# Kernel tuning notes

Hardware: AMD Instinct MI355X
Metric: run time of the kernel (lower is better)

## Reference

```python
import jax, jax.numpy as jnp
import numpy as np

N, E, DIN, GB, GD, LB, LD, G = 50000, 640000, 64, 128, 4, 256, 2, 1024


def setup_inputs() -> dict:
    key = jax.random.key(0)
    ks = jax.random.split(key, 20)
    p = lambda k, shape: (jax.random.normal(k, shape, dtype=jnp.float32) * 0.05)
    return {
        "x": jax.random.normal(ks[0], (N, DIN), dtype=jnp.float32),
        "edge_index": jax.random.randint(ks[1], (2, E), 0, N, dtype=jnp.int64),
        "batch": jnp.sort(jax.random.randint(ks[2], (N,), 0, G, dtype=jnp.int64)),
        "num_graphs": G,
        "W0": p(ks[3], (DIN, GB)), "b0": p(ks[4], (GB,)),
        "Wg": p(ks[5], (GD, GB, GB)), "bg": p(ks[6], (GD, GB)),
        "gamma_g": jnp.ones((GD, GB), jnp.float32), "beta_g": jnp.zeros((GD, GB), jnp.float32),
        "Wl0": p(ks[7], (GB, LB)), "bl0": p(ks[8], (LB,)),
        "Wl": p(ks[9], (LD, LB, LB)), "bl": p(ks[10], (LD, LB)),
        "gamma_l": jnp.ones((LD, LB), jnp.float32), "beta_l": jnp.zeros((LD, LB), jnp.float32),
        "Wout": p(ks[11], (LB, 2)), "bout": p(ks[12], (2,)),
    }


def reference(x, edge_index, batch, num_graphs, W0, b0, Wg, bg, gamma_g, beta_g,
              Wl0, bl0, Wl, bl, gamma_l, beta_l, Wout, bout):
    n = x.shape[0]
    src, dst = edge_index[0], edge_index[1]
    # GCN degree normalization with self loops: deg = 1 + in-degree
    deg = jax.ops.segment_sum(jnp.ones(src.shape[0], x.dtype), dst, num_segments=n) + 1.0
    dinv = jax.lax.rsqrt(deg)                 # deg^{-1/2}
    enorm = dinv[src] * dinv[dst]             # [E] edge norm
    snorm = dinv * dinv                       # [N] self-loop norm (deg^{-1})

    def gcn(h, W, b):
        hw = h @ W                                            # [N, GB]
        agg = jax.ops.segment_sum(hw[src] * enorm[:, None], dst, num_segments=n)
        return agg + hw * snorm[:, None] + b

    def bn(h, g, bt):  # training-mode batchnorm (biased var), eps=1e-5
        m = h.mean(0)
        v = h.var(0)
        return (h - m) * jax.lax.rsqrt(v + 1e-5) * g + bt

    h = jax.nn.relu(gcn(x, W0, b0))
    for i in range(Wg.shape[0]):
        h = jax.nn.relu(bn(gcn(h, Wg[i], bg[i]), gamma_g[i], beta_g[i]))
    # global_add_pool
    hp = jax.ops.segment_sum(h, batch, num_segments=num_graphs)  # [G, GB]
    h = jax.nn.relu(hp @ Wl0 + bl0)
    for i in range(Wl.shape[0]):
        h = jax.nn.relu(bn(h @ Wl[i] + bl[i], gamma_l[i], beta_l[i]))
    return h @ Wout + bout
```

## Files before the change

### kernel.cpp

```cpp
#include <hip/hip_runtime.h>

#define NN 50000
#define EE 640000
#define DINv 64
#define GBv 128
#define GDv 4
#define LBv 256
#define LDv 2
#define GGv 1024

#define NB 196
#define BCAP 4096
#define BTILE 4096
#define NBT ((EE + BTILE - 1) / BTILE)

#define NTILES ((NN + 63) / 64)
#define UPN (NN * 16)
#define CONVN (DINv * GBv + GDv * GBv * GBv)

typedef _Float16 f16x8 __attribute__((ext_vector_type(8)));
typedef float f32x4 __attribute__((ext_vector_type(4)));

__device__ __forceinline__ float h2f(ushort u) {
  union { ushort u; _Float16 h; } x;
  x.u = u;
  return (float)x.h;
}
__device__ __forceinline__ ushort f2h(float f) {
  union { ushort u; _Float16 h; } x;
  x.h = (_Float16)f;
  return x.u;
}


__global__ __launch_bounds__(256) void k_bucket(const int* __restrict__ ei,
                                                int* __restrict__ bcnt,
                                                uint* __restrict__ bkt) {
  __shared__ int lcnt[NB];
  __shared__ int lbase[NB];
  __shared__ int gbase[NB];
  __shared__ int ls[256];
  __shared__ uint stage[BTILE];
  __shared__ ushort sb[BTILE];
  int tid = threadIdx.x;
  int t0 = blockIdx.x * BTILE;
  int cnt = min(BTILE, EE - t0);
  for (int i = tid; i < NB; i += 256) lcnt[i] = 0;
  __syncthreads();

  uint en[16];
  int bb[16], rk[16];
  int nper = (cnt + 255) >> 8;
  for (int k = 0; k < nper; k++) {
    int e = k * 256 + tid;
    if (e < cnt) {
      int src = ei[t0 + e];
      int dst = ei[EE + t0 + e];
      int b = dst >> 8;
      en[k] = ((uint)src << 8) | (uint)(dst & 255);
      bb[k] = b;
      rk[k] = atomicAdd(&lcnt[b], 1);
    } else {
      bb[k] = -1;
    }
  }
  __syncthreads();

  int v = (tid < NB) ? lcnt[tid] : 0;
  ls[tid] = v;
  __syncthreads();
  for (int off = 1; off < 256; off <<= 1) {
    int t = (tid >= off) ? ls[tid - off] : 0;
    __syncthreads();
    ls[tid] += t;
    __syncthreads();
  }
  if (tid < NB) {
    lbase[tid] = ls[tid] - v;
    gbase[tid] = atomicAdd(&bcnt[tid], v);
  }
  __syncthreads();

  for (int k = 0; k < nper; k++) {
    if (bb[k] >= 0) {
      int slot = lbase[bb[k]] + rk[k];
      stage[slot] = en[k];
      sb[slot] = (ushort)bb[k];
    }
  }
  __syncthreads();

  for (int i = tid; i < cnt; i += 256) {
    int b = sb[i];
    bkt[(size_t)b * BCAP + gbase[b] + (i - lbase[b])] = stage[i];
  }
}

__global__ __launch_bounds__(256) void k_bscan(const int* __restrict__ bcnt,
                                               int* __restrict__ bbase,
                                               int* __restrict__ offs) {
  __shared__ int ls[256];
  int tid = threadIdx.x;
  int v = (tid < NB) ? bcnt[tid] : 0;
  ls[tid] = v;
  __syncthreads();
  for (int off = 1; off < 256; off <<= 1) {
    int t = (tid >= off) ? ls[tid - off] : 0;
    __syncthreads();
    ls[tid] += t;
    __syncthreads();
  }
  if (tid < NB) bbase[tid] = ls[tid] - v;
  if (tid == 0) offs[NN] = EE;
}


__global__ __launch_bounds__(256) void k_csr(const uint* __restrict__ bkt,
                                             const int* __restrict__ bcnt,
                                             const int* __restrict__ bbase,
                                             int* __restrict__ offs,
                                             float* __restrict__ dinv,
                                             int* __restrict__ col,
                                             int* __restrict__ deg,
                                             int* __restrict__ ghist) {
  __shared__ int lhist[256];
  __shared__ int lofs[256];
  __shared__ int lcur[256];
  __shared__ int lh2[64];
  int b = blockIdx.x;
  int cnt = bcnt[b], base = bbase[b];
  const uint* B = bkt + (size_t)b * BCAP;
  int tid = threadIdx.x;
  lhist[tid] = 0;
  if (tid < 64) lh2[tid] = 0;
  __syncthreads();
  for (int i = tid; i < cnt; i += 256) atomicAdd(&lhist[B[i] & 255], 1);
  __syncthreads();
  int v = lhist[tid];
  lofs[tid] = v;
  __syncthreads();
  for (int off = 1; off < 256; off <<= 1) {
    int t = (tid >= off) ? lofs[tid - off] : 0;
    __syncthreads();
    lofs[tid] += t;
    __syncthreads();
  }
  int excl = lofs[tid] - v;
  int n = b * 256 + tid;
  if (n < NN) {
    offs[n] = base + excl;
    dinv[n] = rsqrtf((float)(v + 1));
    int d = min(v, 63);
    deg[n] = d;
    atomicAdd(&lh2[d], 1);
  }
  lcur[tid] = excl;
  __syncthreads();
  if (tid < 64 && lh2[tid]) atomicAdd(&ghist[tid], lh2[tid]);
  for (int i = tid; i < cnt; i += 256) {
    uint e = B[i];
    int p = atomicAdd(&lcur[e & 255], 1);
    col[base + p] = (int)(e >> 8);
  }
}

__global__ void k_dscan(const int* __restrict__ ghist, int* __restrict__ dcur) {
  if (threadIdx.x == 0 && blockIdx.x == 0) {
    int run = 0;
    for (int i = 0; i < 64; i++) {
      dcur[i] = run;
      run += ghist[i];
    }
  }
}

__global__ __launch_bounds__(256) void k_dperm(const int* __restrict__ deg,
                                               int* __restrict__ dcur,
                                               int* __restrict__ perm) {
  __shared__ int lhist[64];
  __shared__ int lbase[64];
  int tid = threadIdx.x;
  if (tid < 64) lhist[tid] = 0;
  __syncthreads();
  int n = blockIdx.x * 256 + tid;
  int d = 0, rk = 0;
  if (n < NN) {
    d = deg[n];
    rk = atomicAdd(&lhist[d], 1);
  }
  __syncthreads();
  if (tid < 64 && lhist[tid]) lbase[tid] = atomicAdd(&dcur[tid], lhist[tid]);
  __syncthreads();
  if (n < NN) perm[lbase[d] + rk] = n;
}


__global__ __launch_bounds__(256) void k_prep(const float* __restrict__ x,
                                              const float* __restrict__ dinv,
                                              const float* __restrict__ W0,
                                              const float* __restrict__ Wg,
                                              ushort* __restrict__ u,
                                              ushort* __restrict__ Wt0,
                                              ushort* __restrict__ Wtg) {
  int idx = blockIdx.x * 256 + threadIdx.x;
  if (idx < UPN) {
    int n = idx >> 4;
    float4 v = ((const float4*)x)[idx];
    float d = dinv[n];
    union { ushort us[4]; uint2 q; } o;
    o.us[0] = f2h(v.x * d);
    o.us[1] = f2h(v.y * d);
    o.us[2] = f2h(v.z * d);
    o.us[3] = f2h(v.w * d);
    ((uint2*)u)[idx] = o.q;
  } else {
    int j = idx - UPN;
    if (j < DINv * GBv) {
      int c = j >> 6, k = j & 63;
      Wt0[j] = f2h(W0[k * GBv + c]);
    } else if (j < CONVN) {
      int e = j - DINv * GBv;
      int i = e >> 14, rem = e & 16383;
      int c = rem >> 7, k = rem & 127;
      Wtg[e] = f2h(Wg[i * GBv * GBv + k * GBv + c]);
    }
  }
}


template <int K, int MODE>
__global__ __launch_bounds__(256) void k_agg(const ushort* __restrict__ Gin,
                                             const int* __restrict__ col,
                                             const int* __restrict__ offs,
                                             const float* __restrict__ dinv,
                                             const int* __restrict__ perm,
                                             const float* __restrict__ st,
                                             const float* __restrict__ gamma,
                                             const float* __restrict__ beta,
                                             ushort* __restrict__ V) {
  constexpr int VEC = K / 16;
  __shared__ float sS[128], sT[128];
  int tid = threadIdx.x;
  if constexpr (MODE == 2) {
    if (tid < 128) {
      float mu = st[tid] * (1.f / NN);
      float var = st[128 + tid] * (1.f / NN) - mu * mu;
      float s = rsqrtf(var + 1e-5f) * gamma[tid];
      sS[tid] = s;
      sT[tid] = beta[tid] - mu * s;
    }
    __syncthreads();
  }
  int lane = tid & 63;
  int q = lane >> 4, m = lane & 15;
  int idx = blockIdx.x * 16 + (tid >> 6) * 4 + q;
  int n = perm[idx];

  float sc[VEC], tc[VEC];
  if constexpr (MODE == 2) {
#pragma unroll
    for (int v = 0; v < VEC; v++) {
      sc[v] = sS[m * VEC + v];
      tc[v] = sT[m * VEC + v];
    }
  }

  union U { uint4 v4; uint2 v2; ushort us[8]; };
  auto loadrow = [&](int s) {
    U u;
    const ushort* p = Gin + (long)s * K + m * VEC;
    if constexpr (VEC == 8) u.v4 = *(const uint4*)p;
    else u.v2 = *(const uint2*)p;
    return u;
  };
  float acc[VEC];
#pragma unroll
  for (int v = 0; v < VEC; v++) acc[v] = 0.f;
  auto addrow = [&](U u, float dv) {
#pragma unroll
    for (int v = 0; v < VEC; v++) {
      float g = h2f(u.us[v]);
      if constexpr (MODE == 0) acc[v] += g;
      else if constexpr (MODE == 1) acc[v] += fmaxf(g, 0.f) * dv;
      else acc[v] += fmaxf(g * sc[v] + tc[v], 0.f) * dv;
    }
  };

  float dn = dinv[n];
  addrow(loadrow(n), dn);

  int s0 = offs[n], s1 = offs[n + 1];
  int j = s0;
  for (; j + 7 < s1; j += 8) {
    int si[8];
#pragma unroll
    for (int t = 0; t < 8; t++) si[t] = col[j + t];
    U uu[8];
#pragma unroll
    for (int t = 0; t < 8; t++) uu[t] = loadrow(si[t]);
    float dd[8];
#pragma unroll
    for (int t = 0; t < 8; t++) dd[t] = (MODE != 0) ? dinv[si[t]] : 0.f;
#pragma unroll
    for (int t = 0; t < 8; t++) addrow(uu[t], dd[t]);
  }
  for (; j + 3 < s1; j += 4) {
    int si[4];
#pragma unroll
    for (int t = 0; t < 4; t++) si[t] = col[j + t];
    U uu[4];
#pragma unroll
    for (int t = 0; t < 4; t++) uu[t] = loadrow(si[t]);
    float dd[4];
#pragma unroll
    for (int t = 0; t < 4; t++) dd[t] = (MODE != 0) ? dinv[si[t]] : 0.f;
#pragma unroll
    for (int t = 0; t < 4; t++) addrow(uu[t], dd[t]);
  }
  for (; j < s1; j++) {
    int s = col[j];
    U u = loadrow(s);
    float dv = (MODE != 0) ? dinv[s] : 0.f;
    addrow(u, dv);
  }

  U o;
#pragma unroll
  for (int v = 0; v < VEC; v++) o.us[v] = f2h(acc[v] * dn);
  ushort* op = V + (long)n * K + m * VEC;
  if constexpr (VEC == 8) *(uint4*)op = o.v4;
  else *(uint2*)op = o.v2;
}


template <int K, bool STATS>
__global__ __launch_bounds__(256) void k_mm(const ushort* __restrict__ X,
                                            const ushort* __restrict__ Wt,
                                            const float* __restrict__ bias,
                                            float* __restrict__ stG,
                                            ushort* __restrict__ Gout) {
  constexpr int KP = K + 8;
  constexpr int CP = 136;
  constexpr bool REUSE = (K == 128);
  __shared__ __attribute__((aligned(16))) _Float16 sW[128 * KP];
  __shared__ __attribute__((aligned(16))) _Float16 sA[64 * KP];
  __shared__ __attribute__((aligned(16))) _Float16 sCbuf[REUSE ? 8 : 64 * CP];
  __shared__ float sB[128];
  __shared__ float ssum[128], ssq[128];
  _Float16* sC = REUSE ? sA : sCbuf;
  int tid = threadIdx.x;

  {
    constexpr int CH = K / 8;
    for (int i = tid; i < 128 * CH; i += 256) {
      int c = i / CH, ch = i - c * CH;
      *(uint4*)&sW[c * KP + ch * 8] = ((const uint4*)Wt)[i];
    }
  }
  if (tid < 128) {
    sB[tid] = bias[tid];
    if constexpr (STATS) {
      ssum[tid] = 0.f;
      ssq[tid] = 0.f;
    }
  }

  int w = tid >> 6, lane = tid & 63;
  int m = lane & 15, quad = lane >> 4;
  int crow = 16 * w + quad * 4;

  float ps[8], pq[8];
  if constexpr (STATS) {
#pragma unroll
    for (int ct = 0; ct < 8; ct++) { ps[ct] = 0.f; pq[ct] = 0.f; }
  }

  for (int tile = blockIdx.x; tile < NTILES; tile += gridDim.x) {
    int row0 = tile * 64;
    __syncthreads();

    {
      int r = tid >> 2, col0 = (tid & 3) * (K / 4);
      int gr = row0 + r;
      const uint4* p = (const uint4*)(X + (long)gr * K + col0);
#pragma unroll
      for (int ch = 0; ch < K / 32; ch++) {
        uint4 v = (gr < NN) ? p[ch] : make_uint4(0, 0, 0, 0);
        *(uint4*)&sA[r * KP + col0 + ch * 8] = v;
      }
    }
    __syncthreads();

    f32x4 acc[8];
#pragma unroll
    for (int ct = 0; ct < 8; ct++) acc[ct] = (f32x4){0.f, 0.f, 0.f, 0.f};
    const _Float16* pa = &sA[(16 * w + m) * KP + quad * 8];
#pragma unroll
    for (int ks = 0; ks < K; ks += 32) {
      f16x8 a = *(const f16x8*)(pa + ks);
#pragma unroll
      for (int ct = 0; ct < 8; ct++) {
        f16x8 b = *(const f16x8*)&sW[(ct * 16 + m) * KP + ks + quad * 8];
        acc[ct] = __builtin_amdgcn_mfma_f32_16x16x32_f16(a, b, acc[ct], 0, 0, 0);
      }
    }

    if constexpr (STATS) {
#pragma unroll
      for (int ct = 0; ct < 8; ct++) {
        int c = ct * 16 + m;
        float b = sB[c];
#pragma unroll
        for (int r = 0; r < 4; r++) {
          if (row0 + crow + r < NN) {
            float g = acc[ct][r] + b;
            ps[ct] += g;
            pq[ct] += g * g;
          }
        }
      }
    }
    if constexpr (REUSE) __syncthreads();

#pragma unroll
    for (int ct = 0; ct < 8; ct++) {
      int c = ct * 16 + m;
      float b = sB[c];
#pragma unroll
      for (int r = 0; r < 4; r++) sC[(crow + r) * CP + c] = (_Float16)(acc[ct][r] + b);
    }
    __syncthreads();

    {
      int r = tid >> 2, col0 = (tid & 3) * 32;
      int gr = row0 + r;
      if (gr < NN) {
        const uint4* src = (const uint4*)&sC[r * CP + col0];
        uint4* dst = (uint4*)(Gout + (long)gr * 128 + col0);
#pragma unroll
        for (int ch = 0; ch < 4; ch++) dst[ch] = src[ch];
      }
    }
  }

  if constexpr (STATS) {
#pragma unroll
    for (int ct = 0; ct < 8; ct++) {
      float s = ps[ct], q = pq[ct];
      s += __shfl_xor(s, 16);
      q += __shfl_xor(q, 16);
      s += __shfl_xor(s, 32);
      q += __shfl_xor(q, 32);
      if (quad == 0) {
        atomicAdd(&ssum[ct * 16 + m], s);
        atomicAdd(&ssq[ct * 16 + m], q);
      }
    }
    __syncthreads();
    if (tid < 128) {
      int c = (tid + blockIdx.x * 8) & 127;
      atomicAdd(&stG[c], ssum[c]);
      atomicAdd(&stG[128 + c], ssq[c]);
    }
  }
}


__global__ __launch_bounds__(128) void k_pool2(const ushort* __restrict__ G,
                                               const float* __restrict__ st,
                                               const float* __restrict__ gamma,
                                               const float* __restrict__ beta,
                                               const int* __restrict__ batch,
                                               float* __restrict__ hp) {
  __shared__ int sse[2];
  int g = blockIdx.x;
  int c = threadIdx.x;
  if (c < 2) {
    int key = g + c;
    int lo = 0, hi = NN;
    while (lo < hi) {
      int mid = (lo + hi) >> 1;
      if (batch[mid] < key) lo = mid + 1;
      else hi = mid;
    }
    sse[c] = lo;
  }
  __syncthreads();
  int s = sse[0], e = sse[1];
  float m = st[c] * (1.f / NN);
  float v = st[128 + c] * (1.f / NN) - m * m;
  float sc = rsqrtf(v + 1e-5f) * gamma[c];
  float tc = beta[c] - m * sc;
  float acc = 0.f;
  for (int n = s; n < e; n++) acc += fmaxf(h2f(G[(long)n * 128 + c]) * sc + tc, 0.f);
  hp[(long)g * 128 + c] = acc;
}


__global__ void k_colstats(const float* __restrict__ X, int rows, float* __restrict__ st) {
  int c = threadIdx.x;
  int C = blockDim.x;
  float s = 0.f, q = 0.f;
  for (int r = blockIdx.x; r < rows; r += gridDim.x) {
    float v = X[(long)r * C + c];
    s += v;
    q += v * v;
  }
  atomicAdd(&st[c], s);
  atomicAdd(&st[C + c], q);
}


template <int KIN, int MODE>
__global__ __launch_bounds__(256) void k_fc(const float* __restrict__ X,
                                            const float* __restrict__ W,
                                            const float* __restrict__ b,
                                            const float* __restrict__ st,
                                            const float* __restrict__ gamma,
                                            const float* __restrict__ beta,
                                            float* __restrict__ Y) {
  __shared__ float sx[KIN];
  int g = blockIdx.x;
  int c = threadIdx.x;
  for (int k = c; k < KIN; k += 256) {
    float v = X[(long)g * KIN + k];
    if constexpr (MODE == 2) {
      float m = st[k] * (1.f / GGv);
      float var = st[KIN + k] * (1.f / GGv) - m * m;
      v = fmaxf((v - m) * rsqrtf(var + 1e-5f) * gamma[k] + beta[k], 0.f);
    }
    sx[k] = v;
  }
  __syncthreads();
  float acc = b[c];
#pragma unroll 8
  for (int k = 0; k < KIN; k++) acc += sx[k] * W[(long)k * 256 + c];
  Y[(long)g * 256 + c] = (MODE == 0) ? fmaxf(acc, 0.f) : acc;
}

__global__ __launch_bounds__(256) void k_out(const float* __restrict__ X,
                                             const float* __restrict__ st,
                                             const float* __restrict__ gamma,
                                             const float* __restrict__ beta,
                                             const float* __restrict__ Wout,
                                             const float* __restrict__ bout,
                                             float* __restrict__ out) {
  int g = blockIdx.x * 4 + (threadIdx.x >> 6);
  int l = threadIdx.x & 63;
  float a0 = 0.f, a1 = 0.f;
  for (int k = l; k < LBv; k += 64) {
    float z = X[(long)g * LBv + k];
    float m = st[k] * (1.f / GGv);
    float var = st[LBv + k] * (1.f / GGv) - m * m;
    float x = fmaxf((z - m) * rsqrtf(var + 1e-5f) * gamma[k] + beta[k], 0.f);
    a0 += x * Wout[2 * k];
    a1 += x * Wout[2 * k + 1];
  }
  for (int off = 32; off > 0; off >>= 1) {
    a0 += __shfl_down(a0, off);
    a1 += __shfl_down(a1, off);
  }
  if (l == 0) {
    out[2 * g] = a0 + bout[0];
    out[2 * g + 1] = a1 + bout[1];
  }
}


extern "C" void kernel_launch(void* const* d_in, const int* in_sizes, int n_in,
                              void* d_out, int out_size, void* d_ws, size_t ws_size,
                              hipStream_t stream) {
  const float* x = (const float*)d_in[0];
  const int* ei = (const int*)d_in[1];
  const int* batch = (const int*)d_in[2];
  const float* W0 = (const float*)d_in[4];
  const float* b0 = (const float*)d_in[5];
  const float* Wg = (const float*)d_in[6];
  const float* bg = (const float*)d_in[7];
  const float* gamma_g = (const float*)d_in[8];
  const float* beta_g = (const float*)d_in[9];
  const float* Wl0 = (const float*)d_in[10];
  const float* bl0 = (const float*)d_in[11];
  const float* Wl = (const float*)d_in[12];
  const float* bl = (const float*)d_in[13];
  const float* gamma_l = (const float*)d_in[14];
  const float* beta_l = (const float*)d_in[15];
  const float* Wout = (const float*)d_in[16];
  const float* bout = (const float*)d_in[17];
  float* out = (float*)d_out;

  char* w = (char*)d_ws;
  auto alloc = [&](size_t bytes) {
    void* p = (void*)w;
    w += (bytes + 255) & ~(size_t)255;
    return p;
  };
  int* bcnt = (int*)alloc((size_t)NB * 4);
  float* stAll = (float*)alloc((size_t)(4 * 256 + 2 * 512) * 4);
  int* ghist = (int*)alloc((size_t)64 * 4);
  size_t zspan = (char*)w - (char*)bcnt;
  uint* bkt = (uint*)alloc((size_t)NB * BCAP * 4);
  int* bbase = (int*)alloc((size_t)NB * 4);
  int* offs = (int*)alloc((size_t)(NN + 1) * 4);
  int* col = (int*)alloc((size_t)EE * 4);
  float* dinv = (float*)alloc((size_t)NN * 4);
  int* deg = (int*)alloc((size_t)NN * 4);
  int* perm = (int*)alloc((size_t)NN * 4);
  int* dcur = (int*)alloc((size_t)64 * 4);
  ushort* u = (ushort*)alloc((size_t)NN * DINv * 2);
  ushort* V = (ushort*)alloc((size_t)NN * GBv * 2);
  ushort* g = (ushort*)alloc((size_t)NN * GBv * 2);
  ushort* Wt0 = (ushort*)alloc((size_t)DINv * GBv * 2);
  ushort* Wtg = (ushort*)alloc((size_t)GDv * GBv * GBv * 2);
  float* hp = (float*)alloc((size_t)GGv * GBv * 4);
  float* m1 = (float*)alloc((size_t)GGv * LBv * 4);
  float* m2 = (float*)alloc((size_t)GGv * LBv * 4);

  float* stg = stAll;
  float* sth0 = stAll + 4 * 256;
  float* sth1 = sth0 + 512;

  hipMemsetAsync(bcnt, 0, zspan, stream);

  k_bucket<<<NBT, 256, 0, stream>>>(ei, bcnt, bkt);
  k_bscan<<<1, 256, 0, stream>>>(bcnt, bbase, offs);
  k_csr<<<NB, 256, 0, stream>>>(bkt, bcnt, bbase, offs, dinv, col, deg, ghist);
  k_dscan<<<1, 64, 0, stream>>>(ghist, dcur);
  k_dperm<<<NB, 256, 0, stream>>>(deg, dcur, perm);
  k_prep<<<(UPN + CONVN + 255) / 256, 256, 0, stream>>>(x, dinv, W0, Wg, u, Wt0, Wtg);

  const int AGG = NN / 16;
  const int MMG = 512;

  k_agg<64, 0><<<AGG, 256, 0, stream>>>(u, col, offs, dinv, perm, nullptr, nullptr,
                                        nullptr, V);
  k_mm<64, false><<<MMG, 256, 0, stream>>>(V, Wt0, b0, nullptr, g);

  k_agg<128, 1><<<AGG, 256, 0, stream>>>(g, col, offs, dinv, perm, nullptr, nullptr,
                                         nullptr, V);
  k_mm<128, true><<<MMG, 256, 0, stream>>>(V, Wtg, bg, stg, g);

  for (int i = 1; i < GDv; i++) {
    k_agg<128, 2><<<AGG, 256, 0, stream>>>(g, col, offs, dinv, perm,
                                           stg + (size_t)(i - 1) * 256,
                                           gamma_g + (size_t)(i - 1) * GBv,
                                           beta_g + (size_t)(i - 1) * GBv, V);
    k_mm<128, true><<<MMG, 256, 0, stream>>>(V, Wtg + (size_t)i * GBv * GBv,
                                             bg + (size_t)i * GBv, stg + (size_t)i * 256, g);
  }

  k_pool2<<<GGv, 128, 0, stream>>>(g, stg + 3 * 256, gamma_g + 3 * GBv, beta_g + 3 * GBv,
                                   batch, hp);

  k_fc<GBv, 0><<<GGv, 256, 0, stream>>>(hp, Wl0, bl0, nullptr, nullptr, nullptr, m1);
  k_fc<LBv, 1><<<GGv, 256, 0, stream>>>(m1, Wl, bl, nullptr, nullptr, nullptr, m2);
  k_colstats<<<256, LBv, 0, stream>>>(m2, GGv, sth0);
  k_fc<LBv, 2><<<GGv, 256, 0, stream>>>(m2, Wl + (size_t)LBv * LBv, bl + LBv, sth0,
                                        gamma_l, beta_l, m1);
  k_colstats<<<256, LBv, 0, stream>>>(m1, GGv, sth1);
  k_out<<<GGv / 4, 256, 0, stream>>>(m1, sth1, gamma_l + LBv, beta_l + LBv, Wout, bout, out);
}
```

Before: 446.8 us.

## Fold tiny scan and column-stat kernels into neighbouring kernels to cut launches

The bucket-count scan is moved into every k_csr block, which now redundantly computes the prefix over all 196 bucket counts. The degree-histogram scan is moved into k_dperm, with the global offset added at write time. The two column-statistics kernels are replaced by atomic accumulation of sum and sum-of-squares inside the FC kernels. This removes four small serial launches at the cost of redundant per-block scans and 2x256 atomics per FC block, which contend on the same addresses.

Measured after the change: 473.8 us. 1.06x slower.

```diff
diff --git a/kernel.cpp b/kernel.cpp
--- a/kernel.cpp
+++ b/kernel.cpp
@@ -96,28 +96,9 @@
   }
 }
 
-__global__ __launch_bounds__(256) void k_bscan(const int* __restrict__ bcnt,
-                                               int* __restrict__ bbase,
-                                               int* __restrict__ offs) {
-  __shared__ int ls[256];
-  int tid = threadIdx.x;
-  int v = (tid < NB) ? bcnt[tid] : 0;
-  ls[tid] = v;
-  __syncthreads();
-  for (int off = 1; off < 256; off <<= 1) {
-    int t = (tid >= off) ? ls[tid - off] : 0;
-    __syncthreads();
-    ls[tid] += t;
-    __syncthreads();
-  }
-  if (tid < NB) bbase[tid] = ls[tid] - v;
-  if (tid == 0) offs[NN] = EE;
-}
-
 
 __global__ __launch_bounds__(256) void k_csr(const uint* __restrict__ bkt,
                                              const int* __restrict__ bcnt,
-                                             const int* __restrict__ bbase,
                                              int* __restrict__ offs,
                                              float* __restrict__ dinv,
                                              int* __restrict__ col,
@@ -127,13 +108,25 @@
   __shared__ int lofs[256];
   __shared__ int lcur[256];
   __shared__ int lh2[64];
+  __shared__ int sbase[256];
   int b = blockIdx.x;
-  int cnt = bcnt[b], base = bbase[b];
-  const uint* B = bkt + (size_t)b * BCAP;
   int tid = threadIdx.x;
+
+  int bv = (tid < NB) ? bcnt[tid] : 0;
+  sbase[tid] = bv;
   lhist[tid] = 0;
   if (tid < 64) lh2[tid] = 0;
   __syncthreads();
+  for (int off = 1; off < 256; off <<= 1) {
+    int t = (tid >= off) ? sbase[tid - off] : 0;
+    __syncthreads();
+    sbase[tid] += t;
+    __syncthreads();
+  }
+  int base = sbase[b] - bcnt[b];
+  int cnt = bcnt[b];
+  const uint* B = bkt + (size_t)b * BCAP;
+
   for (int i = tid; i < cnt; i += 256) atomicAdd(&lhist[B[i] & 255], 1);
   __syncthreads();
   int v = lhist[tid];
@@ -157,6 +150,7 @@
   lcur[tid] = excl;
   __syncthreads();
   if (tid < 64 && lh2[tid]) atomicAdd(&ghist[tid], lh2[tid]);
+  if (b == 0 && tid == 0) offs[NN] = EE;
   for (int i = tid; i < cnt; i += 256) {
     uint e = B[i];
     int p = atomicAdd(&lcur[e & 255], 1);
@@ -164,23 +158,22 @@
   }
 }
 
-__global__ void k_dscan(const int* __restrict__ ghist, int* __restrict__ dcur) {
-  if (threadIdx.x == 0 && blockIdx.x == 0) {
-    int run = 0;
-    for (int i = 0; i < 64; i++) {
-      dcur[i] = run;
-      run += ghist[i];
-    }
-  }
-}
-
 __global__ __launch_bounds__(256) void k_dperm(const int* __restrict__ deg,
-                                               int* __restrict__ dcur,
+                                               const int* __restrict__ ghist,
+                                               int* __restrict__ gcur,
                                                int* __restrict__ perm) {
   __shared__ int lhist[64];
   __shared__ int lbase[64];
+  __shared__ int gbase[64];
   int tid = threadIdx.x;
   if (tid < 64) lhist[tid] = 0;
+  if (tid == 0) {
+    int run = 0;
+    for (int i = 0; i < 64; i++) {
+      gbase[i] = run;
+      run += ghist[i];
+    }
+  }
   __syncthreads();
   int n = blockIdx.x * 256 + tid;
   int d = 0, rk = 0;
@@ -189,9 +182,9 @@
     rk = atomicAdd(&lhist[d], 1);
   }
   __syncthreads();
-  if (tid < 64 && lhist[tid]) lbase[tid] = atomicAdd(&dcur[tid], lhist[tid]);
-  __syncthreads();
-  if (n < NN) perm[lbase[d] + rk] = n;
+  if (tid < 64 && lhist[tid]) lbase[tid] = atomicAdd(&gcur[tid], lhist[tid]);
+  __syncthreads();
+  if (n < NN) perm[gbase[d] + lbase[d] + rk] = n;
 }
 
 
@@ -497,27 +490,14 @@
 }
 
 
-__global__ void k_colstats(const float* __restrict__ X, int rows, float* __restrict__ st) {
-  int c = threadIdx.x;
-  int C = blockDim.x;
-  float s = 0.f, q = 0.f;
-  for (int r = blockIdx.x; r < rows; r += gridDim.x) {
-    float v = X[(long)r * C + c];
-    s += v;
-    q += v * v;
-  }
-  atomicAdd(&st[c], s);
-  atomicAdd(&st[C + c], q);
-}
-
-
-template <int KIN, int MODE>
+template <int KIN, int MODE, bool STATS>
 __global__ __launch_bounds__(256) void k_fc(const float* __restrict__ X,
                                             const float* __restrict__ W,
                                             const float* __restrict__ b,
                                             const float* __restrict__ st,
                                             const float* __restrict__ gamma,
                                             const float* __restrict__ beta,
+                                            float* __restrict__ stOut,
                                             float* __restrict__ Y) {
   __shared__ float sx[KIN];
   int g = blockIdx.x;
@@ -535,7 +515,12 @@
   float acc = b[c];
 #pragma unroll 8
   for (int k = 0; k < KIN; k++) acc += sx[k] * W[(long)k * 256 + c];
-  Y[(long)g * 256 + c] = (MODE == 0) ? fmaxf(acc, 0.f) : acc;
+  float yv = (MODE == 0) ? fmaxf(acc, 0.f) : acc;
+  Y[(long)g * 256 + c] = yv;
+  if constexpr (STATS) {
+    atomicAdd(&stOut[c], yv);
+    atomicAdd(&stOut[256 + c], yv * yv);
+  }
 }
 
 __global__ __launch_bounds__(256) void k_out(const float* __restrict__ X,
@@ -598,15 +583,14 @@
   int* bcnt = (int*)alloc((size_t)NB * 4);
   float* stAll = (float*)alloc((size_t)(4 * 256 + 2 * 512) * 4);
   int* ghist = (int*)alloc((size_t)64 * 4);
+  int* gcur = (int*)alloc((size_t)64 * 4);
   size_t zspan = (char*)w - (char*)bcnt;
   uint* bkt = (uint*)alloc((size_t)NB * BCAP * 4);
-  int* bbase = (int*)alloc((size_t)NB * 4);
   int* offs = (int*)alloc((size_t)(NN + 1) * 4);
   int* col = (int*)alloc((size_t)EE * 4);
   float* dinv = (float*)alloc((size_t)NN * 4);
   int* deg = (int*)alloc((size_t)NN * 4);
   int* perm = (int*)alloc((size_t)NN * 4);
-  int* dcur = (int*)alloc((size_t)64 * 4);
   ushort* u = (ushort*)alloc((size_t)NN * DINv * 2);
   ushort* V = (ushort*)alloc((size_t)NN * GBv * 2);
   ushort* g = (ushort*)alloc((size_t)NN * GBv * 2);
@@ -623,10 +607,8 @@
   hipMemsetAsync(bcnt, 0, zspan, stream);
 
   k_bucket<<<NBT, 256, 0, stream>>>(ei, bcnt, bkt);
-  k_bscan<<<1, 256, 0, stream>>>(bcnt, bbase, offs);
-  k_csr<<<NB, 256, 0, stream>>>(bkt, bcnt, bbase, offs, dinv, col, deg, ghist);
-  k_dscan<<<1, 64, 0, stream>>>(ghist, dcur);
-  k_dperm<<<NB, 256, 0, stream>>>(deg, dcur, perm);
+  k_csr<<<NB, 256, 0, stream>>>(bkt, bcnt, offs, dinv, col, deg, ghist);
+  k_dperm<<<NB, 256, 0, stream>>>(deg, ghist, gcur, perm);
   k_prep<<<(UPN + CONVN + 255) / 256, 256, 0, stream>>>(x, dinv, W0, Wg, u, Wt0, Wtg);
 
   const int AGG = NN / 16;
@@ -652,11 +634,11 @@
   k_pool2<<<GGv, 128, 0, stream>>>(g, stg + 3 * 256, gamma_g + 3 * GBv, beta_g + 3 * GBv,
                                    batch, hp);
 
-  k_fc<GBv, 0><<<GGv, 256, 0, stream>>>(hp, Wl0, bl0, nullptr, nullptr, nullptr, m1);
-  k_fc<LBv, 1><<<GGv, 256, 0, stream>>>(m1, Wl, bl, nullptr, nullptr, nullptr, m2);
-  k_colstats<<<256, LBv, 0, stream>>>(m2, GGv, sth0);
-  k_fc<LBv, 2><<<GGv, 256, 0, stream>>>(m2, Wl + (size_t)LBv * LBv, bl + LBv, sth0,
-                                        gamma_l, beta_l, m1);
-  k_colstats<<<256, LBv, 0, stream>>>(m1, GGv, sth1);
+  k_fc<GBv, 0, false><<<GGv, 256, 0, stream>>>(hp, Wl0, bl0, nullptr, nullptr, nullptr,
+                                               nullptr, m1);
+  k_fc<LBv, 1, true><<<GGv, 256, 0, stream>>>(m1, Wl, bl, nullptr, nullptr, nullptr,
+                                              sth0, m2);
+  k_fc<LBv, 2, true><<<GGv, 256, 0, stream>>>(m2, Wl + (size_t)LBv * LBv, bl + LBv, sth0,
+                                              gamma_l, beta_l, sth1, m1);
   k_out<<<GGv / 4, 256, 0, stream>>>(m1, sth1, gamma_l + LBv, beta_l + LBv, Wout, bout, out);
 }
```
